# Kernel tuning notes

Hardware: AMD Instinct MI355X
Metric: run time of the kernel (lower is better)

The kernel has to match this reference:

```python
import jax, jax.numpy as jnp
import numpy as np

B, S, D, F, E, NS, K = 2, 1024, 1024, 4096, 8, 8, 2
FS = F // NS  # shared-expert hidden size = d_ff // num_shared_experts


def setup_inputs() -> dict:
    key = jax.random.key(0)
    ks = jax.random.split(key, 8)
    scale = 0.02
    return {
        "hidden_states": jax.random.normal(ks[0], (B, S, D), jnp.float32),
        "gate_W": jax.random.normal(ks[1], (E, D), jnp.float32) * scale,
        "w1_e": jax.random.normal(ks[2], (E, D, F), jnp.float32) * scale,
        "w3_e": jax.random.normal(ks[3], (E, D, F), jnp.float32) * scale,
        "w2_e": jax.random.normal(ks[4], (E, F, D), jnp.float32) * scale,
        "w1_s": jax.random.normal(ks[5], (NS, D, FS), jnp.float32) * scale,
        "w3_s": jax.random.normal(ks[6], (NS, D, FS), jnp.float32) * scale,
        "w2_s": jax.random.normal(ks[7], (NS, FS, D), jnp.float32) * scale,
    }


def reference(hidden_states, gate_W, w1_e, w3_e, w2_e, w1_s, w3_s, w2_s):
    b, s, d = hidden_states.shape
    e = gate_W.shape[0]
    flat = hidden_states.reshape(-1, d)            # [T, D]
    T = flat.shape[0]

    # --- gate: softmax over experts, top-k probs scattered (k=0 slot only survives) ---
    logits = (flat @ gate_W.T).astype(jnp.float32)  # [T, E]
    probs = jax.nn.softmax(logits, axis=-1)
    top_v, top_i = jax.lax.top_k(probs, K)          # [T, K]
    gates = jnp.zeros((T, e), probs.dtype).at[jnp.arange(T)[:, None], top_i].set(top_v)

    # --- routed experts: module runs every expert densely on all tokens ---
    g = jax.nn.silu(jnp.einsum('td,edf->etf', flat, w1_e))  # [E, T, F]
    u = jnp.einsum('td,edf->etf', flat, w3_e)
    out_e = jnp.einsum('etf,efd->etd', g * u, w2_e)         # [E, T, D]
    routed = jnp.einsum('te,etd->td', gates, out_e).reshape(b, s, d)

    # --- shared experts (mean over NS experts) ---
    gs = jax.nn.silu(jnp.einsum('bsd,ndf->nbsf', hidden_states, w1_s))
    us = jnp.einsum('bsd,ndf->nbsf', hidden_states, w3_s)
    shared = jnp.einsum('nbsf,nfd->bsd', gs * us, w2_s) / w1_s.shape[0]

    alpha = 0.5
    return alpha * shared + (1.0 - alpha) * routed
```

## Files before the change

### kernel.cpp

```cpp
#include <hip/hip_runtime.h>

#define T 2048
#define D 1024
#define F 4096
#define E 8
#define NS 8
#define FS 512
#define SHB 5120
#define NROWS 7168
#define MT_MAX 56

typedef float floatx4 __attribute__((ext_vector_type(4)));
typedef short short8 __attribute__((ext_vector_type(8)));

__device__ __forceinline__ unsigned short f2bf(float f) {
  unsigned int u = __float_as_uint(f);
  u += 0x7FFF + ((u >> 16) & 1);
  return (unsigned short)(u >> 16);
}

__device__ __forceinline__ void glds16(const void* g, void* l) {
  __builtin_amdgcn_global_load_lds(
      (const __attribute__((address_space(1))) void*)g,
      (__attribute__((address_space(3))) void*)l, 16, 0, 0);
}

__global__ void gate_kernel(const float* __restrict__ x, const float* __restrict__ gW,
                            unsigned short* __restrict__ xb, int* __restrict__ cnt,
                            int* __restrict__ list_tok, float* __restrict__ list_gate) {
  int t = blockIdx.x, tid = threadIdx.x;
  const float* xr = x + (size_t)t * D;
  float acc[E];
#pragma unroll
  for (int e = 0; e < E; ++e) acc[e] = 0.f;
  for (int d = tid; d < D; d += 256) {
    float xv = xr[d];
    xb[(size_t)t * D + d] = f2bf(xv);
#pragma unroll
    for (int e = 0; e < E; ++e) acc[e] += xv * gW[e * D + d];
  }
#pragma unroll
  for (int o = 32; o > 0; o >>= 1)
#pragma unroll
    for (int e = 0; e < E; ++e) acc[e] += __shfl_down(acc[e], o, 64);
  __shared__ float wred[4][E];
  int lane = tid & 63, wv = tid >> 6;
  if (lane == 0)
#pragma unroll
    for (int e = 0; e < E; ++e) wred[wv][e] = acc[e];
  __syncthreads();
  if (tid == 0) {
    float l[E];
#pragma unroll
    for (int e = 0; e < E; ++e) l[e] = wred[0][e] + wred[1][e] + wred[2][e] + wred[3][e];
    int i1 = 0; float m1 = l[0];
    for (int e = 1; e < E; ++e) if (l[e] > m1) { m1 = l[e]; i1 = e; }
    int i2 = -1; float m2 = -3.4e38f;
    for (int e = 0; e < E; ++e) if (e != i1 && l[e] > m2) { m2 = l[e]; i2 = e; }
    float s = 0.f, p[E];
#pragma unroll
    for (int e = 0; e < E; ++e) { p[e] = __expf(l[e] - m1); s += p[e]; }
    float inv = 1.f / s;
    int p1 = atomicAdd(&cnt[i1], 1);
    list_tok[i1 * T + p1] = t; list_gate[i1 * T + p1] = p[i1] * inv;
    int p2 = atomicAdd(&cnt[i2], 1);
    list_tok[i2 * T + p2] = t; list_gate[i2 * T + p2] = p[i2] * inv;
  }
}

__global__ void offsets_kernel(const int* __restrict__ cnt, int* __restrict__ off,
                               int* __restrict__ mt_expert) {
  if (threadIdx.x == 0 && blockIdx.x == 0) {
    int o = 0;
    for (int e = 0; e < E; ++e) { off[e] = o; o += (cnt[e] + 127) & ~127; }
    off[E] = o;
    for (int i = 0; i < MT_MAX; ++i) mt_expert[i] = -1;
    for (int e = 0; e < E; ++e) {
      int t0 = off[e] >> 7, nt = (cnt[e] + 127) >> 7;
      for (int i = 0; i < nt; ++i) mt_expert[t0 + i] = e;
    }
    for (int i = SHB >> 7; i < MT_MAX; ++i) mt_expert[i] = E;
  }
}

__global__ void scatter_kernel(const int* __restrict__ cnt, const int* __restrict__ off,
                               const int* __restrict__ list_tok, const float* __restrict__ list_gate,
                               int* __restrict__ tok_of_row, float* __restrict__ row_scale,
                               int* __restrict__ tok_rows, int* __restrict__ tk) {
  int idx = blockIdx.x * 256 + threadIdx.x;
  int e = idx >> 11, i = idx & (T - 1);
  if (e < E && i < cnt[e]) {
    int row = off[e] + i;
    int t = list_tok[e * T + i];
    tok_of_row[row] = t;
    row_scale[row] = 0.5f * list_gate[e * T + i];
    int k = atomicAdd(&tk[t], 1);
    tok_rows[2 * t + k] = row;
  }
}

__global__ void transpose_cast(const float* __restrict__ in, unsigned short* __restrict__ out,
                               int R, int C) {
  in += (size_t)blockIdx.z * R * C;
  out += (size_t)blockIdx.z * R * C;
  int r0 = blockIdx.y * 32, c0 = blockIdx.x * 32;
  __shared__ float tile[32][33];
  int tid = threadIdx.x;
  {
    int rl = tid >> 3, cl = (tid & 7) * 4;
    float4 v = *(const float4*)(in + (size_t)(r0 + rl) * C + c0 + cl);
    tile[rl][cl] = v.x; tile[rl][cl + 1] = v.y;
    tile[rl][cl + 2] = v.z; tile[rl][cl + 3] = v.w;
  }
  __syncthreads();
  {
    int cl = tid >> 3, rq = (tid & 7) * 4;
    int c = c0 + cl, r = r0 + rq;
    ushort4 v;
    v.x = f2bf(tile[rq][cl]);     v.y = f2bf(tile[rq + 1][cl]);
    v.z = f2bf(tile[rq + 2][cl]); v.w = f2bf(tile[rq + 3][cl]);
    int Rt = R >> 5;
    size_t o = ((size_t)(c >> 7) * Rt + (r >> 5)) * 4096 + (size_t)(c & 127) * 32 + (r & 31);
    *(ushort4*)(out + o) = v;
  }
}

__global__ __launch_bounds__(256, 2) void up_gemm(
    const unsigned short* __restrict__ xb, const unsigned short* __restrict__ W1T,
    const unsigned short* __restrict__ W3T, const unsigned short* __restrict__ W1sT,
    const unsigned short* __restrict__ W3sT, const int* __restrict__ mt_expert,
    const int* __restrict__ tok_of_row, unsigned short* __restrict__ Hb) {
  int mt = blockIdx.y, ntile = blockIdx.x;
  int e = mt_expert[mt];
  if (e < 0) return;
  const unsigned short *B1, *B3;
  if (e < E) {
    B1 = W1T + (size_t)e * F * D;
    B3 = W3T + (size_t)e * F * D;
  } else {
    B1 = W1sT; B3 = W3sT;
  }
  __shared__ unsigned short Al[128 * 32];
  __shared__ unsigned short B1l[128 * 32];
  __shared__ unsigned short B3l[128 * 32];
  int tid = threadIdx.x;
  int lane = tid & 63, wv = tid >> 6, wm = wv >> 1, wn = wv & 1;
  int row16 = lane & 15, quad = lane >> 4;
  int qsw8 = ((lane >> 4) ^ ((lane >> 1) & 3)) * 8;
  int swzb = (tid & ~3) * 16 + (((tid & 3) ^ ((tid >> 3) & 3)) * 16);

  int ar = tid >> 1;
  int hrow_s = mt * 128 + ar;
  int srow = (e < E) ? tok_of_row[hrow_s] : (hrow_s - SHB);
  int ja = (tid & 1) * 2;
  int sa = (tid >> 2) & 3;
  const uint4* aptr = (const uint4*)(xb + (size_t)srow * D) + ja;
  uint4* alds0 = (uint4*)Al + ar * 4 + (ja ^ sa);
  uint4* alds1 = (uint4*)Al + ar * 4 + ((ja + 1) ^ sa);

  const unsigned short* b1t = B1 + (size_t)ntile * (D / 32) * 4096;
  const unsigned short* b3t = B3 + (size_t)ntile * (D / 32) * 4096;

  floatx4 accg[4][4], accu[4][4];
#pragma unroll
  for (int i = 0; i < 4; ++i)
#pragma unroll
    for (int j = 0; j < 4; ++j) {
      accg[i][j] = (floatx4){0.f, 0.f, 0.f, 0.f};
      accu[i][j] = (floatx4){0.f, 0.f, 0.f, 0.f};
    }
  int lw = wv * 1024;
  for (int kt = 0; kt < D / 32; ++kt) {
    uint4 av0 = aptr[0];
    uint4 av1 = aptr[1];
    const char* b1s = (const char*)(b1t + (size_t)kt * 4096);
    const char* b3s = (const char*)(b3t + (size_t)kt * 4096);
    glds16(b1s + swzb, (char*)B1l + lw);
    glds16(b1s + 4096 + swzb, (char*)B1l + 4096 + lw);
    glds16(b3s + swzb, (char*)B3l + lw);
    glds16(b3s + 4096 + swzb, (char*)B3l + 4096 + lw);
    alds0[0] = av0; alds1[0] = av1;
    __syncthreads();
    short8 af[4], b1f[4], b3f[4];
#pragma unroll
    for (int mi = 0; mi < 4; ++mi)
      af[mi] = *(const short8*)(Al + (wm * 64 + mi * 16 + row16) * 32 + qsw8);
#pragma unroll
    for (int ni = 0; ni < 4; ++ni) {
      b1f[ni] = *(const short8*)(B1l + (wn * 64 + ni * 16 + row16) * 32 + qsw8);
      b3f[ni] = *(const short8*)(B3l + (wn * 64 + ni * 16 + row16) * 32 + qsw8);
    }
#pragma unroll
    for (int mi = 0; mi < 4; ++mi)
#pragma unroll
      for (int ni = 0; ni < 4; ++ni) {
        accg[mi][ni] = __builtin_amdgcn_mfma_f32_16x16x32_bf16(af[mi], b1f[ni], accg[mi][ni], 0, 0, 0);
        accu[mi][ni] = __builtin_amdgcn_mfma_f32_16x16x32_bf16(af[mi], b3f[ni], accu[mi][ni], 0, 0, 0);
      }
    aptr += 4;
    __syncthreads();
  }
#pragma unroll
  for (int mi = 0; mi < 4; ++mi)
#pragma unroll
    for (int ni = 0; ni < 4; ++ni)
#pragma unroll
      for (int r = 0; r < 4; ++r) {
        int hrow = mt * 128 + wm * 64 + mi * 16 + quad * 4 + r;
        int col = ntile * 128 + wn * 64 + ni * 16 + row16;
        float g = accg[mi][ni][r], u = accu[mi][ni][r];
        float h = g * u / (1.0f + __expf(-g));
        size_t o = ((size_t)(hrow >> 7) * 128 + (col >> 5)) * 4096 + (size_t)(hrow & 127) * 32 + (col & 31);
        Hb[o] = f2bf(h);
      }
}

__global__ __launch_bounds__(256, 2) void down_gemm(
    const unsigned short* __restrict__ Hb, const unsigned short* __restrict__ W2T,
    const unsigned short* __restrict__ W2sT, const int* __restrict__ mt_expert,
    const float* __restrict__ row_scale, float* __restrict__ O) {
  int mt = blockIdx.y, ntile = blockIdx.x, kz = blockIdx.z;
  int e = mt_expert[mt];
  if (e < 0) return;
  const unsigned short* Bt = ((e < E) ? (W2T + (size_t)e * D * F) : W2sT)
                             + (size_t)ntile * (F / 32) * 4096;
  const unsigned short* At = Hb + (size_t)mt * (F / 32) * 4096;
  O += (size_t)kz * NROWS * D;
  __shared__ unsigned short Al[128 * 32];
  __shared__ unsigned short Bl[128 * 32];
  int tid = threadIdx.x;
  int lane = tid & 63, wv = tid >> 6, wm = wv >> 1, wn = wv & 1;
  int row16 = lane & 15, quad = lane >> 4;
  int qsw8 = ((lane >> 4) ^ ((lane >> 1) & 3)) * 8;
  int swzb = (tid & ~3) * 16 + (((tid & 3) ^ ((tid >> 3) & 3)) * 16);
  floatx4 acc[4][4];
#pragma unroll
  for (int i = 0; i < 4; ++i)
#pragma unroll
    for (int j = 0; j < 4; ++j) acc[i][j] = (floatx4){0.f, 0.f, 0.f, 0.f};
  int lw = wv * 1024;
  for (int kt = kz * 64; kt < kz * 64 + 64; ++kt) {
    const char* as = (const char*)(At + (size_t)kt * 4096);
    const char* bs = (const char*)(Bt + (size_t)kt * 4096);
    glds16(as + swzb, (char*)Al + lw);
    glds16(as + 4096 + swzb, (char*)Al + 4096 + lw);
    glds16(bs + swzb, (char*)Bl + lw);
    glds16(bs + 4096 + swzb, (char*)Bl + 4096 + lw);
    __syncthreads();
    short8 af[4], bf[4];
#pragma unroll
    for (int mi = 0; mi < 4; ++mi)
      af[mi] = *(const short8*)(Al + (wm * 64 + mi * 16 + row16) * 32 + qsw8);
#pragma unroll
    for (int ni = 0; ni < 4; ++ni)
      bf[ni] = *(const short8*)(Bl + (wn * 64 + ni * 16 + row16) * 32 + qsw8);
#pragma unroll
    for (int mi = 0; mi < 4; ++mi)
#pragma unroll
      for (int ni = 0; ni < 4; ++ni)
        acc[mi][ni] = __builtin_amdgcn_mfma_f32_16x16x32_bf16(af[mi], bf[ni], acc[mi][ni], 0, 0, 0);
    __syncthreads();
  }
#pragma unroll
  for (int mi = 0; mi < 4; ++mi)
#pragma unroll
    for (int ni = 0; ni < 4; ++ni)
#pragma unroll
      for (int r = 0; r < 4; ++r) {
        int grow = mt * 128 + wm * 64 + mi * 16 + quad * 4 + r;
        int col = ntile * 128 + wn * 64 + ni * 16 + row16;
        float scale = (grow < SHB) ? row_scale[grow] : 0.0625f;
        O[(size_t)grow * D + col] = acc[mi][ni][r] * scale;
      }
}

__global__ void combine_kernel(const float* __restrict__ O, const int* __restrict__ tok_rows,
                               float* __restrict__ out) {
  int idx = blockIdx.x * 256 + threadIdx.x;
  int t = idx >> 8, c = idx & 255;
  int r0 = tok_rows[2 * t], r1 = tok_rows[2 * t + 1];
  const float4* O4 = (const float4*)O;
  const size_t HLF = (size_t)NROWS * 256;
  float4 a = O4[(size_t)r0 * 256 + c];
  float4 b = O4[(size_t)r1 * 256 + c];
  float4 s = O4[((size_t)SHB + t) * 256 + c];
  float4 a2 = O4[HLF + (size_t)r0 * 256 + c];
  float4 b2 = O4[HLF + (size_t)r1 * 256 + c];
  float4 s2 = O4[HLF + ((size_t)SHB + t) * 256 + c];
  float4 r;
  r.x = a.x + b.x + s.x + a2.x + b2.x + s2.x;
  r.y = a.y + b.y + s.y + a2.y + b2.y + s2.y;
  r.z = a.z + b.z + s.z + a2.z + b2.z + s2.z;
  r.w = a.w + b.w + s.w + a2.w + b2.w + s2.w;
  ((float4*)out)[idx] = r;
}

extern "C" void kernel_launch(void* const* d_in, const int* in_sizes, int n_in,
                              void* d_out, int out_size, void* d_ws, size_t ws_size,
                              hipStream_t stream) {
  (void)in_sizes; (void)n_in; (void)out_size; (void)ws_size;
  const float* x   = (const float*)d_in[0];
  const float* gW  = (const float*)d_in[1];
  const float* w1e = (const float*)d_in[2];
  const float* w3e = (const float*)d_in[3];
  const float* w2e = (const float*)d_in[4];
  const float* w1s = (const float*)d_in[5];
  const float* w3s = (const float*)d_in[6];
  const float* w2s = (const float*)d_in[7];
  float* out = (float*)d_out;

  char* w = (char*)d_ws;
  auto alloc = [&](size_t bytes) {
    char* p = w; w += (bytes + 255) & ~(size_t)255; return p;
  };
  unsigned short* xb   = (unsigned short*)alloc((size_t)T * D * 2);
  unsigned short* W1T  = (unsigned short*)alloc((size_t)E * F * D * 2);
  unsigned short* W3T  = (unsigned short*)alloc((size_t)E * F * D * 2);
  unsigned short* W2T  = (unsigned short*)alloc((size_t)E * D * F * 2);
  unsigned short* W1sT = (unsigned short*)alloc((size_t)F * D * 2);
  unsigned short* W3sT = (unsigned short*)alloc((size_t)F * D * 2);
  unsigned short* W2sT = (unsigned short*)alloc((size_t)D * F * 2);
  unsigned short* Hb   = (unsigned short*)alloc((size_t)NROWS * F * 2);
  float* Ob        = (float*)alloc((size_t)2 * NROWS * D * 4);
  float* row_scale = (float*)alloc((size_t)SHB * 4);
  float* list_gate = (float*)alloc((size_t)E * T * 4);
  int* list_tok    = (int*)alloc((size_t)E * T * 4);
  int* tok_rows    = (int*)alloc((size_t)T * 2 * 4);
  int* offv        = (int*)alloc(16 * 4);
  int* mt_expert   = (int*)alloc(64 * 4);
  int* ctrl        = (int*)alloc((size_t)(8 + T + SHB) * 4);
  int* cnt = ctrl; int* tk = ctrl + 8; int* tok_of_row = ctrl + 8 + T;

  hipMemsetAsync(ctrl, 0, (size_t)(8 + T + SHB) * 4, stream);
  gate_kernel<<<T, 256, 0, stream>>>(x, gW, xb, cnt, list_tok, list_gate);
  offsets_kernel<<<1, 64, 0, stream>>>(cnt, offv, mt_expert);
  scatter_kernel<<<(E * T) / 256, 256, 0, stream>>>(cnt, offv, list_tok, list_gate,
                                                    tok_of_row, row_scale, tok_rows, tk);
  transpose_cast<<<dim3(F / 32, D / 32, E), 256, 0, stream>>>(w1e, W1T, D, F);
  transpose_cast<<<dim3(F / 32, D / 32, E), 256, 0, stream>>>(w3e, W3T, D, F);
  transpose_cast<<<dim3(D / 32, F / 32, E), 256, 0, stream>>>(w2e, W2T, F, D);
  transpose_cast<<<dim3(FS / 32, D / 32, NS), 256, 0, stream>>>(w1s, W1sT, D, FS);
  transpose_cast<<<dim3(FS / 32, D / 32, NS), 256, 0, stream>>>(w3s, W3sT, D, FS);
  transpose_cast<<<dim3(D / 32, F / 32, 1), 256, 0, stream>>>(w2s, W2sT, F, D);
  up_gemm<<<dim3(F / 128, MT_MAX), 256, 0, stream>>>(xb, W1T, W3T, W1sT, W3sT,
                                                     mt_expert, tok_of_row, Hb);
  down_gemm<<<dim3(D / 128, MT_MAX, 2), 256, 0, stream>>>(Hb, W2T, W2sT, mt_expert, row_scale, Ob);
  combine_kernel<<<(T * D / 4) / 256, 256, 0, stream>>>(Ob, tok_rows, out);
}
```

Baseline: 745.2 us.

## Fuse weight transposes, switch to 32x32 MFMA, atomically scatter down-proj output

The six per-weight transpose_cast launches become one transpose_all launch that handles 64x64 tiles and writes 16-byte bf16 stores. Both GEMMs move from 16x16x32 to 32x32x16 bf16 MFMA with matching swizzled LDS reads and epilogue indexing. The grids are reordered so consecutive blocks walk the M tiles. The down GEMM now atomically adds its scaled result straight into the zeroed output, which removes the Ob buffer, tok_rows bookkeeping and the combine kernel. In exchange the output needs an extra memset, float atomics make the summation order nondeterministic, and many atomics hit the same token rows.

```diff
diff --git a/kernel.cpp b/kernel.cpp
--- a/kernel.cpp
+++ b/kernel.cpp
@@ -10,8 +10,8 @@
 #define NROWS 7168
 #define MT_MAX 56
 
-typedef float floatx4 __attribute__((ext_vector_type(4)));
 typedef short short8 __attribute__((ext_vector_type(8)));
+typedef float floatx16 __attribute__((ext_vector_type(16)));
 
 __device__ __forceinline__ unsigned short f2bf(float f) {
   unsigned int u = __float_as_uint(f);
@@ -85,43 +85,56 @@
 
 __global__ void scatter_kernel(const int* __restrict__ cnt, const int* __restrict__ off,
                                const int* __restrict__ list_tok, const float* __restrict__ list_gate,
-                               int* __restrict__ tok_of_row, float* __restrict__ row_scale,
-                               int* __restrict__ tok_rows, int* __restrict__ tk) {
+                               int* __restrict__ tok_of_row, float* __restrict__ row_scale) {
   int idx = blockIdx.x * 256 + threadIdx.x;
   int e = idx >> 11, i = idx & (T - 1);
   if (e < E && i < cnt[e]) {
     int row = off[e] + i;
-    int t = list_tok[e * T + i];
-    tok_of_row[row] = t;
+    tok_of_row[row] = list_tok[e * T + i];
     row_scale[row] = 0.5f * list_gate[e * T + i];
-    int k = atomicAdd(&tk[t], 1);
-    tok_rows[2 * t + k] = row;
-  }
-}
-
-__global__ void transpose_cast(const float* __restrict__ in, unsigned short* __restrict__ out,
-                               int R, int C) {
-  in += (size_t)blockIdx.z * R * C;
-  out += (size_t)blockIdx.z * R * C;
-  int r0 = blockIdx.y * 32, c0 = blockIdx.x * 32;
-  __shared__ float tile[32][33];
+  }
+}
+
+struct TPtrs {
+  const float* src[6];
+  unsigned short* dst[6];
+};
+__global__ void transpose_all(TPtrs p) {
+  int b = blockIdx.x;
+  const float* src; unsigned short* dst;
+  int R, C, csh, sl, t;
+  if (b < 8192)       { src = p.src[0]; dst = p.dst[0]; R = 1024; C = 4096; csh = 6; sl = b >> 10; t = b & 1023; }
+  else if (b < 16384) { b -= 8192;  src = p.src[1]; dst = p.dst[1]; R = 1024; C = 4096; csh = 6; sl = b >> 10; t = b & 1023; }
+  else if (b < 24576) { b -= 16384; src = p.src[2]; dst = p.dst[2]; R = 4096; C = 1024; csh = 4; sl = b >> 10; t = b & 1023; }
+  else if (b < 25600) { b -= 24576; src = p.src[3]; dst = p.dst[3]; R = 1024; C = 512;  csh = 3; sl = b >> 7;  t = b & 127; }
+  else if (b < 26624) { b -= 25600; src = p.src[4]; dst = p.dst[4]; R = 1024; C = 512;  csh = 3; sl = b >> 7;  t = b & 127; }
+  else                { b -= 26624; src = p.src[5]; dst = p.dst[5]; R = 4096; C = 1024; csh = 4; sl = 0;       t = b; }
+  src += (size_t)sl * R * C;
+  dst += (size_t)sl * R * C;
+  int rt = t >> csh, ct = t & ((1 << csh) - 1);
+  int r0 = rt * 64, c0 = ct * 64;
+  __shared__ float tile[64][65];
   int tid = threadIdx.x;
-  {
-    int rl = tid >> 3, cl = (tid & 7) * 4;
-    float4 v = *(const float4*)(in + (size_t)(r0 + rl) * C + c0 + cl);
+#pragma unroll
+  for (int pp = 0; pp < 4; ++pp) {
+    int idx = pp * 256 + tid;
+    int rl = idx >> 4, cl = (idx & 15) * 4;
+    float4 v = *(const float4*)(src + (size_t)(r0 + rl) * C + c0 + cl);
     tile[rl][cl] = v.x; tile[rl][cl + 1] = v.y;
     tile[rl][cl + 2] = v.z; tile[rl][cl + 3] = v.w;
   }
   __syncthreads();
-  {
-    int cl = tid >> 3, rq = (tid & 7) * 4;
-    int c = c0 + cl, r = r0 + rq;
-    ushort4 v;
-    v.x = f2bf(tile[rq][cl]);     v.y = f2bf(tile[rq + 1][cl]);
-    v.z = f2bf(tile[rq + 2][cl]); v.w = f2bf(tile[rq + 3][cl]);
-    int Rt = R >> 5;
+  int Rt = R >> 5;
+#pragma unroll
+  for (int pp = 0; pp < 2; ++pp) {
+    int idx = pp * 256 + tid;
+    int cl = idx >> 3, r8 = (idx & 7) * 8;
+    int c = c0 + cl, r = r0 + r8;
+    short8 v;
+#pragma unroll
+    for (int i = 0; i < 8; ++i) v[i] = (short)f2bf(tile[r8 + i][cl]);
     size_t o = ((size_t)(c >> 7) * Rt + (r >> 5)) * 4096 + (size_t)(c & 127) * 32 + (r & 31);
-    *(ushort4*)(out + o) = v;
+    *(short8*)(dst + o) = v;
   }
 }
 
@@ -130,7 +143,7 @@
     const unsigned short* __restrict__ W3T, const unsigned short* __restrict__ W1sT,
     const unsigned short* __restrict__ W3sT, const int* __restrict__ mt_expert,
     const int* __restrict__ tok_of_row, unsigned short* __restrict__ Hb) {
-  int mt = blockIdx.y, ntile = blockIdx.x;
+  int mt = blockIdx.x, ntile = blockIdx.y;
   int e = mt_expert[mt];
   if (e < 0) return;
   const unsigned short *B1, *B3;
@@ -145,8 +158,9 @@
   __shared__ unsigned short B3l[128 * 32];
   int tid = threadIdx.x;
   int lane = tid & 63, wv = tid >> 6, wm = wv >> 1, wn = wv & 1;
-  int row16 = lane & 15, quad = lane >> 4;
-  int qsw8 = ((lane >> 4) ^ ((lane >> 1) & 3)) * 8;
+  int l31 = lane & 31, lh = lane >> 5;
+  int key = (l31 >> 1) & 3;
+  int slot0 = (lh ^ key) * 8, slot1 = ((2 + lh) ^ key) * 8;
   int swzb = (tid & ~3) * 16 + (((tid & 3) ^ ((tid >> 3) & 3)) * 16);
 
   int ar = tid >> 1;
@@ -161,13 +175,13 @@
   const unsigned short* b1t = B1 + (size_t)ntile * (D / 32) * 4096;
   const unsigned short* b3t = B3 + (size_t)ntile * (D / 32) * 4096;
 
-  floatx4 accg[4][4], accu[4][4];
-#pragma unroll
-  for (int i = 0; i < 4; ++i)
-#pragma unroll
-    for (int j = 0; j < 4; ++j) {
-      accg[i][j] = (floatx4){0.f, 0.f, 0.f, 0.f};
-      accu[i][j] = (floatx4){0.f, 0.f, 0.f, 0.f};
+  floatx16 accg[2][2], accu[2][2];
+#pragma unroll
+  for (int i = 0; i < 2; ++i)
+#pragma unroll
+    for (int j = 0; j < 2; ++j) {
+      accg[i][j] = (floatx16)(0.f);
+      accu[i][j] = (floatx16)(0.f);
     }
   int lw = wv * 1024;
   for (int kt = 0; kt < D / 32; ++kt) {
@@ -181,36 +195,42 @@
     glds16(b3s + 4096 + swzb, (char*)B3l + 4096 + lw);
     alds0[0] = av0; alds1[0] = av1;
     __syncthreads();
-    short8 af[4], b1f[4], b3f[4];
-#pragma unroll
-    for (int mi = 0; mi < 4; ++mi)
-      af[mi] = *(const short8*)(Al + (wm * 64 + mi * 16 + row16) * 32 + qsw8);
-#pragma unroll
-    for (int ni = 0; ni < 4; ++ni) {
-      b1f[ni] = *(const short8*)(B1l + (wn * 64 + ni * 16 + row16) * 32 + qsw8);
-      b3f[ni] = *(const short8*)(B3l + (wn * 64 + ni * 16 + row16) * 32 + qsw8);
-    }
-#pragma unroll
-    for (int mi = 0; mi < 4; ++mi)
-#pragma unroll
-      for (int ni = 0; ni < 4; ++ni) {
-        accg[mi][ni] = __builtin_amdgcn_mfma_f32_16x16x32_bf16(af[mi], b1f[ni], accg[mi][ni], 0, 0, 0);
-        accu[mi][ni] = __builtin_amdgcn_mfma_f32_16x16x32_bf16(af[mi], b3f[ni], accu[mi][ni], 0, 0, 0);
+#pragma unroll
+    for (int s = 0; s < 2; ++s) {
+      int so = s ? slot1 : slot0;
+      short8 af[2], b1f[2], b3f[2];
+#pragma unroll
+      for (int mi = 0; mi < 2; ++mi)
+        af[mi] = *(const short8*)(Al + (wm * 64 + mi * 32 + l31) * 32 + so);
+#pragma unroll
+      for (int ni = 0; ni < 2; ++ni) {
+        int rb = (wn * 64 + ni * 32 + l31) * 32 + so;
+        b1f[ni] = *(const short8*)(B1l + rb);
+        b3f[ni] = *(const short8*)(B3l + rb);
       }
+#pragma unroll
+      for (int mi = 0; mi < 2; ++mi)
+#pragma unroll
+        for (int ni = 0; ni < 2; ++ni) {
+          accg[mi][ni] = __builtin_amdgcn_mfma_f32_32x32x16_bf16(af[mi], b1f[ni], accg[mi][ni], 0, 0, 0);
+          accu[mi][ni] = __builtin_amdgcn_mfma_f32_32x32x16_bf16(af[mi], b3f[ni], accu[mi][ni], 0, 0, 0);
+        }
+    }
     aptr += 4;
     __syncthreads();
   }
 #pragma unroll
-  for (int mi = 0; mi < 4; ++mi)
-#pragma unroll
-    for (int ni = 0; ni < 4; ++ni)
-#pragma unroll
-      for (int r = 0; r < 4; ++r) {
-        int hrow = mt * 128 + wm * 64 + mi * 16 + quad * 4 + r;
-        int col = ntile * 128 + wn * 64 + ni * 16 + row16;
+  for (int mi = 0; mi < 2; ++mi)
+#pragma unroll
+    for (int ni = 0; ni < 2; ++ni)
+#pragma unroll
+      for (int r = 0; r < 16; ++r) {
+        int rowin = (r & 3) + 8 * (r >> 2) + 4 * lh;
+        int hrow = mt * 128 + wm * 64 + mi * 32 + rowin;
+        int col = ntile * 128 + wn * 64 + ni * 32 + l31;
         float g = accg[mi][ni][r], u = accu[mi][ni][r];
         float h = g * u / (1.0f + __expf(-g));
-        size_t o = ((size_t)(hrow >> 7) * 128 + (col >> 5)) * 4096 + (size_t)(hrow & 127) * 32 + (col & 31);
+        size_t o = ((size_t)mt * 128 + (col >> 5)) * 4096 + (size_t)(hrow & 127) * 32 + (col & 31);
         Hb[o] = f2bf(h);
       }
 }
@@ -218,26 +238,27 @@
 __global__ __launch_bounds__(256, 2) void down_gemm(
     const unsigned short* __restrict__ Hb, const unsigned short* __restrict__ W2T,
     const unsigned short* __restrict__ W2sT, const int* __restrict__ mt_expert,
-    const float* __restrict__ row_scale, float* __restrict__ O) {
-  int mt = blockIdx.y, ntile = blockIdx.x, kz = blockIdx.z;
+    const int* __restrict__ tok_of_row, const float* __restrict__ row_scale,
+    float* __restrict__ out) {
+  int mt = blockIdx.x, ntile = blockIdx.y, kz = blockIdx.z;
   int e = mt_expert[mt];
   if (e < 0) return;
   const unsigned short* Bt = ((e < E) ? (W2T + (size_t)e * D * F) : W2sT)
                              + (size_t)ntile * (F / 32) * 4096;
   const unsigned short* At = Hb + (size_t)mt * (F / 32) * 4096;
-  O += (size_t)kz * NROWS * D;
   __shared__ unsigned short Al[128 * 32];
   __shared__ unsigned short Bl[128 * 32];
   int tid = threadIdx.x;
   int lane = tid & 63, wv = tid >> 6, wm = wv >> 1, wn = wv & 1;
-  int row16 = lane & 15, quad = lane >> 4;
-  int qsw8 = ((lane >> 4) ^ ((lane >> 1) & 3)) * 8;
+  int l31 = lane & 31, lh = lane >> 5;
+  int key = (l31 >> 1) & 3;
+  int slot0 = (lh ^ key) * 8, slot1 = ((2 + lh) ^ key) * 8;
   int swzb = (tid & ~3) * 16 + (((tid & 3) ^ ((tid >> 3) & 3)) * 16);
-  floatx4 acc[4][4];
-#pragma unroll
-  for (int i = 0; i < 4; ++i)
-#pragma unroll
-    for (int j = 0; j < 4; ++j) acc[i][j] = (floatx4){0.f, 0.f, 0.f, 0.f};
+  floatx16 acc[2][2];
+#pragma unroll
+  for (int i = 0; i < 2; ++i)
+#pragma unroll
+    for (int j = 0; j < 2; ++j) acc[i][j] = (floatx16)(0.f);
   int lw = wv * 1024;
   for (int kt = kz * 64; kt < kz * 64 + 64; ++kt) {
     const char* as = (const char*)(At + (size_t)kt * 4096);
@@ -247,52 +268,40 @@
     glds16(bs + swzb, (char*)Bl + lw);
     glds16(bs + 4096 + swzb, (char*)Bl + 4096 + lw);
     __syncthreads();
-    short8 af[4], bf[4];
-#pragma unroll
-    for (int mi = 0; mi < 4; ++mi)
-      af[mi] = *(const short8*)(Al + (wm * 64 + mi * 16 + row16) * 32 + qsw8);
-#pragma unroll
-    for (int ni = 0; ni < 4; ++ni)
-      bf[ni] = *(const short8*)(Bl + (wn * 64 + ni * 16 + row16) * 32 + qsw8);
-#pragma unroll
-    for (int mi = 0; mi < 4; ++mi)
-#pragma unroll
-      for (int ni = 0; ni < 4; ++ni)
-        acc[mi][ni] = __builtin_amdgcn_mfma_f32_16x16x32_bf16(af[mi], bf[ni], acc[mi][ni], 0, 0, 0);
+#pragma unroll
+    for (int s = 0; s < 2; ++s) {
+      int so = s ? slot1 : slot0;
+      short8 af[2], bf[2];
+#pragma unroll
+      for (int mi = 0; mi < 2; ++mi)
+        af[mi] = *(const short8*)(Al + (wm * 64 + mi * 32 + l31) * 32 + so);
+#pragma unroll
+      for (int ni = 0; ni < 2; ++ni)
+        bf[ni] = *(const short8*)(Bl + (wn * 64 + ni * 32 + l31) * 32 + so);
+#pragma unroll
+      for (int mi = 0; mi < 2; ++mi)
+#pragma unroll
+        for (int ni = 0; ni < 2; ++ni)
+          acc[mi][ni] = __builtin_amdgcn_mfma_f32_32x32x16_bf16(af[mi], bf[ni], acc[mi][ni], 0, 0, 0);
+    }
     __syncthreads();
   }
 #pragma unroll
-  for (int mi = 0; mi < 4; ++mi)
-#pragma unroll
-    for (int ni = 0; ni < 4; ++ni)
-#pragma unroll
-      for (int r = 0; r < 4; ++r) {
-        int grow = mt * 128 + wm * 64 + mi * 16 + quad * 4 + r;
-        int col = ntile * 128 + wn * 64 + ni * 16 + row16;
-        float scale = (grow < SHB) ? row_scale[grow] : 0.0625f;
-        O[(size_t)grow * D + col] = acc[mi][ni][r] * scale;
+  for (int mi = 0; mi < 2; ++mi)
+#pragma unroll
+    for (int r = 0; r < 16; ++r) {
+      int rowin = (r & 3) + 8 * (r >> 2) + 4 * lh;
+      int grow = mt * 128 + wm * 64 + mi * 32 + rowin;
+      int tok; float scale;
+      if (grow < SHB) { tok = tok_of_row[grow]; scale = row_scale[grow]; }
+      else            { tok = grow - SHB;       scale = 0.0625f; }
+      float* orow = out + (size_t)tok * D;
+#pragma unroll
+      for (int ni = 0; ni < 2; ++ni) {
+        int col = ntile * 128 + wn * 64 + ni * 32 + l31;
+        unsafeAtomicAdd(orow + col, acc[mi][ni][r] * scale);
       }
-}
-
-__global__ void combine_kernel(const float* __restrict__ O, const int* __restrict__ tok_rows,
-                               float* __restrict__ out) {
-  int idx = blockIdx.x * 256 + threadIdx.x;
-  int t = idx >> 8, c = idx & 255;
-  int r0 = tok_rows[2 * t], r1 = tok_rows[2 * t + 1];
-  const float4* O4 = (const float4*)O;
-  const size_t HLF = (size_t)NROWS * 256;
-  float4 a = O4[(size_t)r0 * 256 + c];
-  float4 b = O4[(size_t)r1 * 256 + c];
-  float4 s = O4[((size_t)SHB + t) * 256 + c];
-  float4 a2 = O4[HLF + (size_t)r0 * 256 + c];
-  float4 b2 = O4[HLF + (size_t)r1 * 256 + c];
-  float4 s2 = O4[HLF + ((size_t)SHB + t) * 256 + c];
-  float4 r;
-  r.x = a.x + b.x + s.x + a2.x + b2.x + s2.x;
-  r.y = a.y + b.y + s.y + a2.y + b2.y + s2.y;
-  r.z = a.z + b.z + s.z + a2.z + b2.z + s2.z;
-  r.w = a.w + b.w + s.w + a2.w + b2.w + s2.w;
-  ((float4*)out)[idx] = r;
+    }
 }
 
 extern "C" void kernel_launch(void* const* d_in, const int* in_sizes, int n_in,
@@ -301,12 +310,6 @@
   (void)in_sizes; (void)n_in; (void)out_size; (void)ws_size;
   const float* x   = (const float*)d_in[0];
   const float* gW  = (const float*)d_in[1];
-  const float* w1e = (const float*)d_in[2];
-  const float* w3e = (const float*)d_in[3];
-  const float* w2e = (const float*)d_in[4];
-  const float* w1s = (const float*)d_in[5];
-  const float* w3s = (const float*)d_in[6];
-  const float* w2s = (const float*)d_in[7];
   float* out = (float*)d_out;
 
   char* w = (char*)d_ws;
@@ -321,29 +324,31 @@
   unsigned short* W3sT = (unsigned short*)alloc((size_t)F * D * 2);
   unsigned short* W2sT = (unsigned short*)alloc((size_t)D * F * 2);
   unsigned short* Hb   = (unsigned short*)alloc((size_t)NROWS * F * 2);
-  float* Ob        = (float*)alloc((size_t)2 * NROWS * D * 4);
-  float* row_scale = (float*)alloc((size_t)SHB * 4);
   float* list_gate = (float*)alloc((size_t)E * T * 4);
   int* list_tok    = (int*)alloc((size_t)E * T * 4);
-  int* tok_rows    = (int*)alloc((size_t)T * 2 * 4);
   int* offv        = (int*)alloc(16 * 4);
   int* mt_expert   = (int*)alloc(64 * 4);
-  int* ctrl        = (int*)alloc((size_t)(8 + T + SHB) * 4);
-  int* cnt = ctrl; int* tk = ctrl + 8; int* tok_of_row = ctrl + 8 + T;
-
-  hipMemsetAsync(ctrl, 0, (size_t)(8 + T + SHB) * 4, stream);
+  int* ctrl        = (int*)alloc((size_t)(8 + SHB + SHB) * 4);
+  int* cnt = ctrl;
+  int* tok_of_row  = ctrl + 8;
+  float* row_scale = (float*)(ctrl + 8 + SHB);
+
+  hipMemsetAsync(ctrl, 0, (size_t)(8 + SHB + SHB) * 4, stream);
+  hipMemsetAsync(out, 0, (size_t)T * D * 4, stream);
   gate_kernel<<<T, 256, 0, stream>>>(x, gW, xb, cnt, list_tok, list_gate);
   offsets_kernel<<<1, 64, 0, stream>>>(cnt, offv, mt_expert);
   scatter_kernel<<<(E * T) / 256, 256, 0, stream>>>(cnt, offv, list_tok, list_gate,
-                                                    tok_of_row, row_scale, tok_rows, tk);
-  transpose_cast<<<dim3(F / 32, D / 32, E), 256, 0, stream>>>(w1e, W1T, D, F);
-  transpose_cast<<<dim3(F / 32, D / 32, E), 256, 0, stream>>>(w3e, W3T, D, F);
-  transpose_cast<<<dim3(D / 32, F / 32, E), 256, 0, stream>>>(w2e, W2T, F, D);
-  transpose_cast<<<dim3(FS / 32, D / 32, NS), 256, 0, stream>>>(w1s, W1sT, D, FS);
-  transpose_cast<<<dim3(FS / 32, D / 32, NS), 256, 0, stream>>>(w3s, W3sT, D, FS);
-  transpose_cast<<<dim3(D / 32, F / 32, 1), 256, 0, stream>>>(w2s, W2sT, F, D);
-  up_gemm<<<dim3(F / 128, MT_MAX), 256, 0, stream>>>(xb, W1T, W3T, W1sT, W3sT,
+                                                    tok_of_row, row_scale);
+  TPtrs tp;
+  tp.src[0] = (const float*)d_in[2]; tp.dst[0] = W1T;
+  tp.src[1] = (const float*)d_in[3]; tp.dst[1] = W3T;
+  tp.src[2] = (const float*)d_in[4]; tp.dst[2] = W2T;
+  tp.src[3] = (const float*)d_in[5]; tp.dst[3] = W1sT;
+  tp.src[4] = (const float*)d_in[6]; tp.dst[4] = W3sT;
+  tp.src[5] = (const float*)d_in[7]; tp.dst[5] = W2sT;
+  transpose_all<<<27648, 256, 0, stream>>>(tp);
+  up_gemm<<<dim3(MT_MAX, F / 128), 256, 0, stream>>>(xb, W1T, W3T, W1sT, W3sT,
                                                      mt_expert, tok_of_row, Hb);
-  down_gemm<<<dim3(D / 128, MT_MAX, 2), 256, 0, stream>>>(Hb, W2T, W2sT, mt_expert, row_scale, Ob);
-  combine_kernel<<<(T * D / 4) / 256, 256, 0, stream>>>(Ob, tok_rows, out);
-}
+  down_gemm<<<dim3(MT_MAX, D / 128, 2), 256, 0, stream>>>(Hb, W2T, W2sT, mt_expert,
+                                                          tok_of_row, row_scale, out);
+}
```

Measured after the change: 794.9 us. 1.07x slower.
